# Kernel optimization log

Hardware: AMD Instinct MI355X
Metric: run time of the kernel (lower is better)

The kernel has to match this reference:

```python
import jax, jax.numpy as jnp
import numpy as np

H = 4  # heads (init_kwargs)
E = 64  # embed_size
D = E // H
PREC_DIM = 2
FF = 4 * E


def _layernorm(x, g, b, eps=1e-5):
    mu = jnp.mean(x, axis=-1, keepdims=True)
    var = jnp.mean((x - mu) ** 2, axis=-1, keepdims=True)
    return (x - mu) * jax.lax.rsqrt(var + eps) * g + b


def setup_inputs() -> dict:
    key = jax.random.key(0)
    ks = jax.random.split(key, 16)
    B, S, N = 128, 192, 32
    s = 0.05
    return {
        "precedence": jax.random.normal(ks[0], (B, S, N, PREC_DIM), dtype=jnp.float32),
        "top_mask": jax.random.randint(ks[1], (B, N), 0, 2, dtype=jnp.int32),
        "We": jax.random.normal(ks[2], (PREC_DIM, E), dtype=jnp.float32) * s,
        "be": jnp.zeros((E,), jnp.float32),
        "Wq": jax.random.normal(ks[3], (D, D), dtype=jnp.float32) * s,
        "Wk": jax.random.normal(ks[4], (D, D), dtype=jnp.float32) * s,
        "Wv": jax.random.normal(ks[5], (D, D), dtype=jnp.float32) * s,
        "Wo": jax.random.normal(ks[6], (E, E), dtype=jnp.float32) * s,
        "bo": jnp.zeros((E,), jnp.float32),
        "ln1_g": jnp.ones((E,), jnp.float32),
        "ln1_b": jnp.zeros((E,), jnp.float32),
        "W1": jax.random.normal(ks[7], (E, FF), dtype=jnp.float32) * s,
        "b1": jnp.zeros((FF,), jnp.float32),
        "W2": jax.random.normal(ks[8], (FF, E), dtype=jnp.float32) * s,
        "b2": jnp.zeros((E,), jnp.float32),
        "ln2_g": jnp.ones((E,), jnp.float32),
        "ln2_b": jnp.zeros((E,), jnp.float32),
    }


def reference(precedence, top_mask, We, be, Wq, Wk, Wv, Wo, bo,
              ln1_g, ln1_b, W1, b1, W2, b2, ln2_g, ln2_b):
    B, S, N, _ = precedence.shape
    M = B * S
    # embedding: [B,S,N,E]
    pv = precedence @ We + be
    # gather-indexed query: prec_vecs[:, s, s % box_num]
    sidx = jnp.arange(S)
    q = pv[:, sidx, sidx % N]                      # [B,S,E]
    vals = pv.reshape(M, N, E)                     # values == keys
    qr = q.reshape(M, 1, E)
    # mask: [B,1,1,N] expanded over states -> [M,1,1,N]
    mask = jnp.broadcast_to(top_mask[:, None, None, None, :], (B, S, 1, 1, N)).reshape(M, 1, 1, N)
    # per-head linear projections (shared across heads)
    vh = vals.reshape(M, N, H, D) @ Wv
    kh = vals.reshape(M, N, H, D) @ Wk
    qh = qr.reshape(M, 1, H, D) @ Wq
    energy = jnp.einsum("mqhd,mkhd->mhqk", qh, kh)           # [M,H,1,N]
    energy = jnp.where(mask == 0, jnp.float32(-1e20), energy)
    attn = jax.nn.softmax(energy / jnp.sqrt(jnp.float32(E)), axis=-1)
    oh = jnp.einsum("mhqk,mkhd->mqhd", attn, vh).reshape(M, 1, E)
    ao = oh @ Wo + bo
    x = _layernorm(ao + qr, ln1_g, ln1_b)
    ff = jax.nn.relu(x @ W1 + b1) @ W2 + b2
    out = _layernorm(ff + x, ln2_g, ln2_b)
    return out.reshape(B, S, E)
```

## Files before the change

### kernel.cpp

```cpp
#include <hip/hip_runtime.h>
#include <math.h>

namespace {

constexpr int S_  = 192;
constexpr int TPW = 8;
constexpr int WVB = 4;

__device__ __forceinline__ void wave_fence() {
  asm volatile("s_waitcnt lgkmcnt(0)" ::: "memory");
}

__launch_bounds__(256, 4)
__global__ void prec_fused(
    const float* __restrict__ prec,  const int*   __restrict__ tmask,
    const float* __restrict__ We,    const float* __restrict__ be,
    const float* __restrict__ Wq,    const float* __restrict__ Wk,
    const float* __restrict__ Wv,    const float* __restrict__ Wo,
    const float* __restrict__ bo,    const float* __restrict__ g1,
    const float* __restrict__ bb1,   const float* __restrict__ W1,
    const float* __restrict__ b1,    const float* __restrict__ W2,
    const float* __restrict__ b2,    const float* __restrict__ g2,
    const float* __restrict__ bb2,   float* __restrict__ out)
{
  __shared__ __align__(16) float scratch[WVB][2048];
  __shared__ __align__(16) float sxoh[WVB][TPW][64];

  const int tid  = threadIdx.x;
  const int wv   = tid >> 6;
  const int lane = tid & 63;
  const int u    = lane >> 5;
  const int n    = lane & 31;
  const int tokbase = (blockIdx.x * WVB + wv) * TPW;
  const int bidx0 = tokbase / S_;
  const int srow0 = tokbase - bidx0 * S_;

  float* __restrict__ sc = scratch[wv];

  const bool masked = (tmask[bidx0 * 32 + n] == 0);

  sc[lane]       = We[lane];
  sc[64 + lane]  = We[64 + lane];
  sc[128 + lane] = be[lane];
  #pragma unroll
  for (int i = 0; i < 4; ++i) {
    sc[192 + lane + 64*i] = Wq[lane + 64*i];
    sc[448 + lane + 64*i] = Wk[lane + 64*i];
    sc[704 + lane + 64*i] = Wv[lane + 64*i];
  }
  wave_fence();

  {
    const int h = lane >> 4, c = lane & 15;
    float Te[3] = {0,0,0}, Ke[3] = {0,0,0}, Ve[3] = {0,0,0};
    #pragma unroll
    for (int dp = 0; dp < 16; ++dp) {
      const float u0 = sc[h*16 + dp];
      const float u1 = sc[64 + h*16 + dp];
      const float u2 = sc[128 + h*16 + dp];
      const float wq = sc[192 + dp*16 + c];
      const float wk = sc[448 + dp*16 + c];
      const float wvv = sc[704 + dp*16 + c];
      Te[0] = fmaf(u0, wq, Te[0]); Te[1] = fmaf(u1, wq, Te[1]); Te[2] = fmaf(u2, wq, Te[2]);
      Ke[0] = fmaf(u0, wk, Ke[0]); Ke[1] = fmaf(u1, wk, Ke[1]); Ke[2] = fmaf(u2, wk, Ke[2]);
      Ve[0] = fmaf(u0, wvv, Ve[0]); Ve[1] = fmaf(u1, wvv, Ve[1]); Ve[2] = fmaf(u2, wvv, Ve[2]);
    }
    float Mp[9];
    #pragma unroll
    for (int a = 0; a < 3; ++a)
      #pragma unroll
      for (int b = 0; b < 3; ++b)
        Mp[a*3+b] = Te[a] * Ke[b];
    #pragma unroll
    for (int o = 1; o < 16; o <<= 1) {
      #pragma unroll
      for (int i = 0; i < 9; ++i) Mp[i] += __shfl_xor(Mp[i], o, 64);
    }
    #pragma unroll
    for (int a = 0; a < 3; ++a) sc[960 + (h*3 + a)*16 + c] = Ve[a];
    if (c == 0) {
      #pragma unroll
      for (int i = 0; i < 9; ++i) sc[1152 + h*9 + i] = Mp[i];
    }
  }
  wave_fence();

  float m0[9], m1[9];
  #pragma unroll
  for (int i = 0; i < 9; ++i) {
    m0[i] = sc[1152 + (2*u)*9 + i];
    m1[i] = sc[1152 + (2*u + 1)*9 + i];
  }
  float gO0[3] = {0,0,0}, gO1[3] = {0,0,0}, gT0[3] = {0,0,0}, gT1[3] = {0,0,0};
  {
    const int hoA = 2*u, hoB = 2*u + 1, htA = 2*(1 - u), htB = htA + 1;
    #pragma unroll
    for (int dp = 0; dp < 16; ++dp) {
      const float woA = Wo[(hoA*16 + dp)*64 + lane];
      const float woB = Wo[(hoB*16 + dp)*64 + lane];
      const float woC = Wo[(htA*16 + dp)*64 + lane];
      const float woD = Wo[(htB*16 + dp)*64 + lane];
      #pragma unroll
      for (int a = 0; a < 3; ++a) {
        gO0[a] = fmaf(sc[960 + (hoA*3 + a)*16 + dp], woA, gO0[a]);
        gO1[a] = fmaf(sc[960 + (hoB*3 + a)*16 + dp], woB, gO1[a]);
        gT0[a] = fmaf(sc[960 + (htA*3 + a)*16 + dp], woC, gT0[a]);
        gT1[a] = fmaf(sc[960 + (htB*3 + a)*16 + dp], woD, gT1[a]);
      }
    }
  }
  const float we0l = sc[lane], we1l = sc[64 + lane], bel = sc[128 + lane];
  const float bo_l = bo[lane], g1l = g1[lane], b1l_ = bb1[lane];
  wave_fence();

  #pragma unroll 1
  for (int p = 0; p < TPW; ++p) {
    const int m     = tokbase + p;
    const int nstar = (srow0 + p) & 31;

    const float qx = prec[(size_t)m * 64 + nstar * 2];
    const float qy = prec[(size_t)m * 64 + nstar * 2 + 1];
    const float2 pin = *(const float2*)(prec + (size_t)m * 64 + n * 2);

    const float cA0 = fmaf(qy, m0[3], fmaf(qx, m0[0], m0[6]));
    const float cB0 = fmaf(qy, m0[4], fmaf(qx, m0[1], m0[7]));
    const float cC0 = fmaf(qy, m0[5], fmaf(qx, m0[2], m0[8]));
    const float cA1 = fmaf(qy, m1[3], fmaf(qx, m1[0], m1[6]));
    const float cB1 = fmaf(qy, m1[4], fmaf(qx, m1[1], m1[7]));
    const float cC1 = fmaf(qy, m1[5], fmaf(qx, m1[2], m1[8]));

    const float en0 = fmaf(pin.y, cB0, fmaf(pin.x, cA0, cC0)) * 0.125f;
    const float en1 = fmaf(pin.y, cB1, fmaf(pin.x, cA1, cC1)) * 0.125f;

    const float pe0 = masked ? 0.f : __expf(en0);
    const float pe1 = masked ? 0.f : __expf(en1);
    float s0 = pe0, s1 = pe1;
    #pragma unroll
    for (int o = 1; o < 32; o <<= 1) {
      s0 += __shfl_xor(s0, o, 64);
      s1 += __shfl_xor(s1, o, 64);
    }
    const float w0 = (s0 > 0.f) ? pe0 / s0 : 0.03125f;
    const float w1 = (s1 > 0.f) ? pe1 / s1 : 0.03125f;

    float r0 = w0 * pin.x, r1 = w0 * pin.y, r2 = w0;
    float r3 = w1 * pin.x, r4 = w1 * pin.y, r5 = w1;
    #pragma unroll
    for (int o = 1; o < 32; o <<= 1) {
      r0 += __shfl_xor(r0, o, 64); r1 += __shfl_xor(r1, o, 64);
      r2 += __shfl_xor(r2, o, 64); r3 += __shfl_xor(r3, o, 64);
      r4 += __shfl_xor(r4, o, 64); r5 += __shfl_xor(r5, o, 64);
    }
    const float o0 = __shfl_xor(r0, 32, 64), o1 = __shfl_xor(r1, 32, 64);
    const float o2 = __shfl_xor(r2, 32, 64), o3 = __shfl_xor(r3, 32, 64);
    const float o4 = __shfl_xor(r4, 32, 64), o5 = __shfl_xor(r5, 32, 64);

    float v = bo_l;
    v = fmaf(r0, gO0[0], v); v = fmaf(r1, gO0[1], v); v = fmaf(r2, gO0[2], v);
    v = fmaf(r3, gO1[0], v); v = fmaf(r4, gO1[1], v); v = fmaf(r5, gO1[2], v);
    v = fmaf(o0, gT0[0], v); v = fmaf(o1, gT0[1], v); v = fmaf(o2, gT0[2], v);
    v = fmaf(o3, gT1[0], v); v = fmaf(o4, gT1[1], v); v = fmaf(o5, gT1[2], v);
    v += fmaf(qy, we1l, fmaf(qx, we0l, bel));

    float sm = v, s2 = v * v;
    #pragma unroll
    for (int o = 1; o < 64; o <<= 1) {
      sm += __shfl_xor(sm, o, 64);
      s2 += __shfl_xor(s2, o, 64);
    }
    const float mu  = sm * (1.f/64.f);
    const float var = s2 * (1.f/64.f) - mu * mu;
    const float rs  = rsqrtf(var + 1e-5f);
    sxoh[wv][p][lane] = (v - mu) * rs * g1l + b1l_;
  }
  wave_fence();

  float hacc[TPW][4];
  #pragma unroll
  for (int k = 0; k < 4; ++k) {
    const float bk = b1[lane + 64*k];
    #pragma unroll
    for (int t = 0; t < TPW; ++t) hacc[t][k] = bk;
  }
  #pragma unroll 4
  for (int e4 = 0; e4 < 16; ++e4) {
    float wr[4][4];
    #pragma unroll
    for (int kk = 0; kk < 4; ++kk)
      #pragma unroll
      for (int k = 0; k < 4; ++k)
        wr[kk][k] = W1[(e4*4 + kk)*256 + lane + 64*k];
    #pragma unroll
    for (int t = 0; t < TPW; ++t) {
      const float4 xv = *(const float4*)&sxoh[wv][t][e4*4];
      #pragma unroll
      for (int k = 0; k < 4; ++k) {
        hacc[t][k] = fmaf(xv.x, wr[0][k], hacc[t][k]);
        hacc[t][k] = fmaf(xv.y, wr[1][k], hacc[t][k]);
        hacc[t][k] = fmaf(xv.z, wr[2][k], hacc[t][k]);
        hacc[t][k] = fmaf(xv.w, wr[3][k], hacc[t][k]);
      }
    }
  }
  float* __restrict__ h1buf = sc;
  #pragma unroll
  for (int t = 0; t < TPW; ++t)
    #pragma unroll
    for (int k = 0; k < 4; ++k)
      h1buf[t*256 + lane + 64*k] = fmaxf(hacc[t][k], 0.f);
  wave_fence();

  const int tg = lane >> 5;
  const int e0 = (lane & 31) * 2;
  float f2a[4][2];
  {
    const float2 b2v = *(const float2*)(b2 + e0);
    #pragma unroll
    for (int i = 0; i < 4; ++i) { f2a[i][0] = b2v.x; f2a[i][1] = b2v.y; }
  }
  const float* __restrict__ hb = h1buf + tg * 4 * 256;
  #pragma unroll 8
  for (int f4 = 0; f4 < 64; ++f4) {
    float4 hv[4];
    #pragma unroll
    for (int i = 0; i < 4; ++i)
      hv[i] = *(const float4*)(hb + i*256 + f4*4);
    float2 w2r[4];
    #pragma unroll
    for (int ff = 0; ff < 4; ++ff)
      w2r[ff] = *(const float2*)(W2 + (f4*4 + ff)*64 + e0);
    #pragma unroll
    for (int i = 0; i < 4; ++i) {
      f2a[i][0] = fmaf(hv[i].x, w2r[0].x, f2a[i][0]);
      f2a[i][1] = fmaf(hv[i].x, w2r[0].y, f2a[i][1]);
      f2a[i][0] = fmaf(hv[i].y, w2r[1].x, f2a[i][0]);
      f2a[i][1] = fmaf(hv[i].y, w2r[1].y, f2a[i][1]);
      f2a[i][0] = fmaf(hv[i].z, w2r[2].x, f2a[i][0]);
      f2a[i][1] = fmaf(hv[i].z, w2r[2].y, f2a[i][1]);
      f2a[i][0] = fmaf(hv[i].w, w2r[3].x, f2a[i][0]);
      f2a[i][1] = fmaf(hv[i].w, w2r[3].y, f2a[i][1]);
    }
  }

  {
    const float2 g2v  = *(const float2*)(g2 + e0);
    const float2 bb2v = *(const float2*)(bb2 + e0);
    #pragma unroll
    for (int i = 0; i < 4; ++i) {
      const int t = tg * 4 + i;
      const float2 xv = *(const float2*)&sxoh[wv][t][e0];
      const float v0 = f2a[i][0] + xv.x;
      const float v1 = f2a[i][1] + xv.y;
      float sm = v0 + v1, s2 = v0*v0 + v1*v1;
      #pragma unroll
      for (int o = 1; o < 32; o <<= 1) {
        sm += __shfl_xor(sm, o, 64);
        s2 += __shfl_xor(s2, o, 64);
      }
      const float mu  = sm * (1.f/64.f);
      const float var = s2 * (1.f/64.f) - mu * mu;
      const float rs  = rsqrtf(var + 1e-5f);
      float2 o2;
      o2.x = (v0 - mu) * rs * g2v.x + bb2v.x;
      o2.y = (v1 - mu) * rs * g2v.y + bb2v.y;
      *(float2*)(out + (size_t)(tokbase + t) * 64 + e0) = o2;
    }
  }
}

}

extern "C" void kernel_launch(void* const* d_in, const int* in_sizes, int n_in,
                              void* d_out, int out_size, void* d_ws, size_t ws_size,
                              hipStream_t stream) {
  (void)in_sizes; (void)n_in; (void)d_ws; (void)ws_size; (void)out_size;
  const float* prec = (const float*)d_in[0];
  const int*   tm   = (const int*)  d_in[1];
  const float* We   = (const float*)d_in[2];
  const float* be   = (const float*)d_in[3];
  const float* Wq   = (const float*)d_in[4];
  const float* Wk   = (const float*)d_in[5];
  const float* Wv   = (const float*)d_in[6];
  const float* Wo   = (const float*)d_in[7];
  const float* bo   = (const float*)d_in[8];
  const float* g1   = (const float*)d_in[9];
  const float* bb1  = (const float*)d_in[10];
  const float* W1   = (const float*)d_in[11];
  const float* b1   = (const float*)d_in[12];
  const float* W2   = (const float*)d_in[13];
  const float* b2   = (const float*)d_in[14];
  const float* g2   = (const float*)d_in[15];
  const float* bb2  = (const float*)d_in[16];

  dim3 grid(768), block(256);
  hipLaunchKernelGGL(prec_fused, grid, block, 0, stream,
                     prec, tm, We, be, Wq, Wk, Wv, Wo, bo, g1, bb1,
                     W1, b1, W2, b2, g2, bb2, (float*)d_out);
}
```

Before: 143.5 us.

## Halve tokens per wave, share weight precompute across block, defer softmax normalization

Tokens per wave drop from 8 to 4, the grid doubles, and launch bounds target 6 blocks per CU with a smaller shared buffer, to raise occupancy. The per-wave redundant computation of the folded Q/K/V/Wo weights now runs once per block, split across all 256 threads and joined with __syncthreads. Softmax normalization moves after the reductions using reciprocals of the summed weights, and the bias term for the constant component is folded into one constant, which removes the separate sum shuffle. The new path adds block-level barriers and a uniform all-masked branch, and uses approximate reciprocals.

```diff
diff --git a/kernel.cpp b/kernel.cpp
--- a/kernel.cpp
+++ b/kernel.cpp
@@ -4,14 +4,14 @@
 namespace {
 
 constexpr int S_  = 192;
-constexpr int TPW = 8;
+constexpr int TPW = 4;
 constexpr int WVB = 4;
 
 __device__ __forceinline__ void wave_fence() {
   asm volatile("s_waitcnt lgkmcnt(0)" ::: "memory");
 }
 
-__launch_bounds__(256, 4)
+__launch_bounds__(256, 6)
 __global__ void prec_fused(
     const float* __restrict__ prec,  const int*   __restrict__ tmask,
     const float* __restrict__ We,    const float* __restrict__ be,
@@ -23,7 +23,7 @@
     const float* __restrict__ b2,    const float* __restrict__ g2,
     const float* __restrict__ bb2,   float* __restrict__ out)
 {
-  __shared__ __align__(16) float scratch[WVB][2048];
+  __shared__ __align__(16) float sh[WVB][1040];
   __shared__ __align__(16) float sxoh[WVB][TPW][64];
 
   const int tid  = threadIdx.x;
@@ -35,85 +35,84 @@
   const int bidx0 = tokbase / S_;
   const int srow0 = tokbase - bidx0 * S_;
 
-  float* __restrict__ sc = scratch[wv];
-
+  float* __restrict__ sc = &sh[0][0];
+
+  if (tid < 64) { sc[tid] = We[tid]; sc[64 + tid] = We[64 + tid]; sc[128 + tid] = be[tid]; }
+  sc[192 + tid] = Wq[tid];
+  sc[448 + tid] = Wk[tid];
+  sc[704 + tid] = Wv[tid];
+  __syncthreads();
+
+  {
+    const int sel = tid >> 6;
+    if (sel < 3) {
+      const int h = (tid >> 4) & 3, c = tid & 15;
+      const float* Wm = sc + 192 + sel * 256;
+      float a0 = 0.f, a1 = 0.f, a2 = 0.f;
+      #pragma unroll
+      for (int dp = 0; dp < 16; ++dp) {
+        const float w = Wm[dp * 16 + c];
+        a0 = fmaf(sc[h * 16 + dp],        w, a0);
+        a1 = fmaf(sc[64 + h * 16 + dp],   w, a1);
+        a2 = fmaf(sc[128 + h * 16 + dp],  w, a2);
+      }
+      const int base = 960 + sel * 192 + h * 48 + c;
+      sc[base] = a0; sc[base + 16] = a1; sc[base + 32] = a2;
+    }
+  }
+  __syncthreads();
+
+  if (tid < 36) {
+    const int h = tid / 9, ab = tid - h * 9, a = ab / 3, b = ab - a * 3;
+    const float* Tp = sc + 960  + h * 48 + a * 16;
+    const float* Kp = sc + 1152 + h * 48 + b * 16;
+    float s = 0.f;
+    #pragma unroll
+    for (int c = 0; c < 16; ++c) s = fmaf(Tp[c], Kp[c], s);
+    sc[1536 + tid] = s;
+  }
+  {
+    const int e = tid & 63, h = tid >> 6;
+    const float* Vp = sc + 1344 + h * 48;
+    float q0 = 0.f, q1 = 0.f, q2 = 0.f;
+    #pragma unroll
+    for (int dp = 0; dp < 16; ++dp) {
+      const float wo = Wo[(h * 16 + dp) * 64 + e];
+      q0 = fmaf(Vp[dp],      wo, q0);
+      q1 = fmaf(Vp[16 + dp], wo, q1);
+      q2 = fmaf(Vp[32 + dp], wo, q2);
+    }
+    sc[1600 + (h * 3 + 0) * 64 + e] = q0;
+    sc[1600 + (h * 3 + 1) * 64 + e] = q1;
+    sc[1600 + (h * 3 + 2) * 64 + e] = q2;
+  }
+  __syncthreads();
+
+  float m0[9], m1[9];
+  #pragma unroll
+  for (int i = 0; i < 9; ++i) {
+    m0[i] = sc[1536 + (2 * u) * 9 + i];
+    m1[i] = sc[1536 + (2 * u + 1) * 9 + i];
+  }
+  const int hoA = 2 * u, hoB = 2 * u + 1, htA = 2 - 2 * u, htB = 3 - 2 * u;
+  float gO0[2], gO1[2], gT0[2], gT1[2];
+  #pragma unroll
+  for (int a = 0; a < 2; ++a) {
+    gO0[a] = sc[1600 + (hoA * 3 + a) * 64 + lane];
+    gO1[a] = sc[1600 + (hoB * 3 + a) * 64 + lane];
+    gT0[a] = sc[1600 + (htA * 3 + a) * 64 + lane];
+    gT1[a] = sc[1600 + (htB * 3 + a) * 64 + lane];
+  }
+  float c0 = bo[lane];
+  #pragma unroll
+  for (int h = 0; h < 4; ++h) c0 += sc[1600 + (h * 3 + 2) * 64 + lane];
+  const float we0l = sc[lane], we1l = sc[64 + lane], bel = sc[128 + lane];
+  const float g1l = g1[lane], b1l_ = bb1[lane];
   const bool masked = (tmask[bidx0 * 32 + n] == 0);
-
-  sc[lane]       = We[lane];
-  sc[64 + lane]  = We[64 + lane];
-  sc[128 + lane] = be[lane];
-  #pragma unroll
-  for (int i = 0; i < 4; ++i) {
-    sc[192 + lane + 64*i] = Wq[lane + 64*i];
-    sc[448 + lane + 64*i] = Wk[lane + 64*i];
-    sc[704 + lane + 64*i] = Wv[lane + 64*i];
-  }
-  wave_fence();
-
-  {
-    const int h = lane >> 4, c = lane & 15;
-    float Te[3] = {0,0,0}, Ke[3] = {0,0,0}, Ve[3] = {0,0,0};
-    #pragma unroll
-    for (int dp = 0; dp < 16; ++dp) {
-      const float u0 = sc[h*16 + dp];
-      const float u1 = sc[64 + h*16 + dp];
-      const float u2 = sc[128 + h*16 + dp];
-      const float wq = sc[192 + dp*16 + c];
-      const float wk = sc[448 + dp*16 + c];
-      const float wvv = sc[704 + dp*16 + c];
-      Te[0] = fmaf(u0, wq, Te[0]); Te[1] = fmaf(u1, wq, Te[1]); Te[2] = fmaf(u2, wq, Te[2]);
-      Ke[0] = fmaf(u0, wk, Ke[0]); Ke[1] = fmaf(u1, wk, Ke[1]); Ke[2] = fmaf(u2, wk, Ke[2]);
-      Ve[0] = fmaf(u0, wvv, Ve[0]); Ve[1] = fmaf(u1, wvv, Ve[1]); Ve[2] = fmaf(u2, wvv, Ve[2]);
-    }
-    float Mp[9];
-    #pragma unroll
-    for (int a = 0; a < 3; ++a)
-      #pragma unroll
-      for (int b = 0; b < 3; ++b)
-        Mp[a*3+b] = Te[a] * Ke[b];
-    #pragma unroll
-    for (int o = 1; o < 16; o <<= 1) {
-      #pragma unroll
-      for (int i = 0; i < 9; ++i) Mp[i] += __shfl_xor(Mp[i], o, 64);
-    }
-    #pragma unroll
-    for (int a = 0; a < 3; ++a) sc[960 + (h*3 + a)*16 + c] = Ve[a];
-    if (c == 0) {
-      #pragma unroll
-      for (int i = 0; i < 9; ++i) sc[1152 + h*9 + i] = Mp[i];
-    }
-  }
-  wave_fence();
-
-  float m0[9], m1[9];
-  #pragma unroll
-  for (int i = 0; i < 9; ++i) {
-    m0[i] = sc[1152 + (2*u)*9 + i];
-    m1[i] = sc[1152 + (2*u + 1)*9 + i];
-  }
-  float gO0[3] = {0,0,0}, gO1[3] = {0,0,0}, gT0[3] = {0,0,0}, gT1[3] = {0,0,0};
-  {
-    const int hoA = 2*u, hoB = 2*u + 1, htA = 2*(1 - u), htB = htA + 1;
-    #pragma unroll
-    for (int dp = 0; dp < 16; ++dp) {
-      const float woA = Wo[(hoA*16 + dp)*64 + lane];
-      const float woB = Wo[(hoB*16 + dp)*64 + lane];
-      const float woC = Wo[(htA*16 + dp)*64 + lane];
-      const float woD = Wo[(htB*16 + dp)*64 + lane];
-      #pragma unroll
-      for (int a = 0; a < 3; ++a) {
-        gO0[a] = fmaf(sc[960 + (hoA*3 + a)*16 + dp], woA, gO0[a]);
-        gO1[a] = fmaf(sc[960 + (hoB*3 + a)*16 + dp], woB, gO1[a]);
-        gT0[a] = fmaf(sc[960 + (htA*3 + a)*16 + dp], woC, gT0[a]);
-        gT1[a] = fmaf(sc[960 + (htB*3 + a)*16 + dp], woD, gT1[a]);
-      }
-    }
-  }
-  const float we0l = sc[lane], we1l = sc[64 + lane], bel = sc[128 + lane];
-  const float bo_l = bo[lane], g1l = g1[lane], b1l_ = bb1[lane];
-  wave_fence();
-
-  #pragma unroll 1
+  const bool allm   = (__all((int)masked) != 0);
+  __syncthreads();
+
+  #pragma unroll 2
   for (int p = 0; p < TPW; ++p) {
     const int m     = tokbase + p;
     const int nstar = (srow0 + p) & 31;
@@ -128,23 +127,18 @@
     const float cA1 = fmaf(qy, m1[3], fmaf(qx, m1[0], m1[6]));
     const float cB1 = fmaf(qy, m1[4], fmaf(qx, m1[1], m1[7]));
     const float cC1 = fmaf(qy, m1[5], fmaf(qx, m1[2], m1[8]));
-
     const float en0 = fmaf(pin.y, cB0, fmaf(pin.x, cA0, cC0)) * 0.125f;
     const float en1 = fmaf(pin.y, cB1, fmaf(pin.x, cA1, cC1)) * 0.125f;
 
-    const float pe0 = masked ? 0.f : __expf(en0);
-    const float pe1 = masked ? 0.f : __expf(en1);
-    float s0 = pe0, s1 = pe1;
-    #pragma unroll
-    for (int o = 1; o < 32; o <<= 1) {
-      s0 += __shfl_xor(s0, o, 64);
-      s1 += __shfl_xor(s1, o, 64);
-    }
-    const float w0 = (s0 > 0.f) ? pe0 / s0 : 0.03125f;
-    const float w1 = (s1 > 0.f) ? pe1 / s1 : 0.03125f;
-
-    float r0 = w0 * pin.x, r1 = w0 * pin.y, r2 = w0;
-    float r3 = w1 * pin.x, r4 = w1 * pin.y, r5 = w1;
+    float pe0, pe1;
+    if (allm) { pe0 = 1.f; pe1 = 1.f; }
+    else {
+      pe0 = masked ? 0.f : __expf(en0);
+      pe1 = masked ? 0.f : __expf(en1);
+    }
+
+    float r0 = pe0 * pin.x, r1 = pe0 * pin.y, r2 = pe0;
+    float r3 = pe1 * pin.x, r4 = pe1 * pin.y, r5 = pe1;
     #pragma unroll
     for (int o = 1; o < 32; o <<= 1) {
       r0 += __shfl_xor(r0, o, 64); r1 += __shfl_xor(r1, o, 64);
@@ -154,12 +148,14 @@
     const float o0 = __shfl_xor(r0, 32, 64), o1 = __shfl_xor(r1, 32, 64);
     const float o2 = __shfl_xor(r2, 32, 64), o3 = __shfl_xor(r3, 32, 64);
     const float o4 = __shfl_xor(r4, 32, 64), o5 = __shfl_xor(r5, 32, 64);
-
-    float v = bo_l;
-    v = fmaf(r0, gO0[0], v); v = fmaf(r1, gO0[1], v); v = fmaf(r2, gO0[2], v);
-    v = fmaf(r3, gO1[0], v); v = fmaf(r4, gO1[1], v); v = fmaf(r5, gO1[2], v);
-    v = fmaf(o0, gT0[0], v); v = fmaf(o1, gT0[1], v); v = fmaf(o2, gT0[2], v);
-    v = fmaf(o3, gT1[0], v); v = fmaf(o4, gT1[1], v); v = fmaf(o5, gT1[2], v);
+    const float i0 = __builtin_amdgcn_rcpf(r2), i1 = __builtin_amdgcn_rcpf(r5);
+    const float i2 = __builtin_amdgcn_rcpf(o2), i3 = __builtin_amdgcn_rcpf(o5);
+
+    float v = c0;
+    v = fmaf(fmaf(r1, gO0[1], r0 * gO0[0]), i0, v);
+    v = fmaf(fmaf(r4, gO1[1], r3 * gO1[0]), i1, v);
+    v = fmaf(fmaf(o1, gT0[1], o0 * gT0[0]), i2, v);
+    v = fmaf(fmaf(o4, gT1[1], o3 * gT1[0]), i3, v);
     v += fmaf(qy, we1l, fmaf(qx, we0l, bel));
 
     float sm = v, s2 = v * v;
@@ -168,8 +164,8 @@
       sm += __shfl_xor(sm, o, 64);
       s2 += __shfl_xor(s2, o, 64);
     }
-    const float mu  = sm * (1.f/64.f);
-    const float var = s2 * (1.f/64.f) - mu * mu;
+    const float mu  = sm * (1.f / 64.f);
+    const float var = s2 * (1.f / 64.f) - mu * mu;
     const float rs  = rsqrtf(var + 1e-5f);
     sxoh[wv][p][lane] = (v - mu) * rs * g1l + b1l_;
   }
@@ -178,7 +174,7 @@
   float hacc[TPW][4];
   #pragma unroll
   for (int k = 0; k < 4; ++k) {
-    const float bk = b1[lane + 64*k];
+    const float bk = b1[lane + 64 * k];
     #pragma unroll
     for (int t = 0; t < TPW; ++t) hacc[t][k] = bk;
   }
@@ -189,10 +185,10 @@
     for (int kk = 0; kk < 4; ++kk)
       #pragma unroll
       for (int k = 0; k < 4; ++k)
-        wr[kk][k] = W1[(e4*4 + kk)*256 + lane + 64*k];
+        wr[kk][k] = W1[(e4 * 4 + kk) * 256 + lane + 64 * k];
     #pragma unroll
     for (int t = 0; t < TPW; ++t) {
-      const float4 xv = *(const float4*)&sxoh[wv][t][e4*4];
+      const float4 xv = *(const float4*)&sxoh[wv][t][e4 * 4];
       #pragma unroll
       for (int k = 0; k < 4; ++k) {
         hacc[t][k] = fmaf(xv.x, wr[0][k], hacc[t][k]);
@@ -202,63 +198,58 @@
       }
     }
   }
-  float* __restrict__ h1buf = sc;
+  float* __restrict__ h1buf = sh[wv];
   #pragma unroll
   for (int t = 0; t < TPW; ++t)
     #pragma unroll
     for (int k = 0; k < 4; ++k)
-      h1buf[t*256 + lane + 64*k] = fmaxf(hacc[t][k], 0.f);
+      h1buf[t * 256 + lane + 64 * k] = fmaxf(hacc[t][k], 0.f);
   wave_fence();
 
   const int tg = lane >> 5;
   const int e0 = (lane & 31) * 2;
-  float f2a[4][2];
+  float f2a[2][2];
   {
     const float2 b2v = *(const float2*)(b2 + e0);
-    #pragma unroll
-    for (int i = 0; i < 4; ++i) { f2a[i][0] = b2v.x; f2a[i][1] = b2v.y; }
-  }
-  const float* __restrict__ hb = h1buf + tg * 4 * 256;
+    f2a[0][0] = b2v.x; f2a[0][1] = b2v.y;
+    f2a[1][0] = b2v.x; f2a[1][1] = b2v.y;
+  }
+  const float* __restrict__ hb = h1buf + tg * 2 * 256;
   #pragma unroll 8
   for (int f4 = 0; f4 < 64; ++f4) {
-    float4 hv[4];
-    #pragma unroll
-    for (int i = 0; i < 4; ++i)
-      hv[i] = *(const float4*)(hb + i*256 + f4*4);
-    float2 w2r[4];
-    #pragma unroll
-    for (int ff = 0; ff < 4; ++ff)
-      w2r[ff] = *(const float2*)(W2 + (f4*4 + ff)*64 + e0);
-    #pragma unroll
-    for (int i = 0; i < 4; ++i) {
-      f2a[i][0] = fmaf(hv[i].x, w2r[0].x, f2a[i][0]);
-      f2a[i][1] = fmaf(hv[i].x, w2r[0].y, f2a[i][1]);
-      f2a[i][0] = fmaf(hv[i].y, w2r[1].x, f2a[i][0]);
-      f2a[i][1] = fmaf(hv[i].y, w2r[1].y, f2a[i][1]);
-      f2a[i][0] = fmaf(hv[i].z, w2r[2].x, f2a[i][0]);
-      f2a[i][1] = fmaf(hv[i].z, w2r[2].y, f2a[i][1]);
-      f2a[i][0] = fmaf(hv[i].w, w2r[3].x, f2a[i][0]);
-      f2a[i][1] = fmaf(hv[i].w, w2r[3].y, f2a[i][1]);
-    }
+    const float4 hv0 = *(const float4*)(hb + f4 * 4);
+    const float4 hv1 = *(const float4*)(hb + 256 + f4 * 4);
+    const float2 w0 = *(const float2*)(W2 + (f4 * 4 + 0) * 64 + e0);
+    const float2 w1 = *(const float2*)(W2 + (f4 * 4 + 1) * 64 + e0);
+    const float2 w2 = *(const float2*)(W2 + (f4 * 4 + 2) * 64 + e0);
+    const float2 w3 = *(const float2*)(W2 + (f4 * 4 + 3) * 64 + e0);
+    f2a[0][0] = fmaf(hv0.x, w0.x, f2a[0][0]); f2a[0][1] = fmaf(hv0.x, w0.y, f2a[0][1]);
+    f2a[0][0] = fmaf(hv0.y, w1.x, f2a[0][0]); f2a[0][1] = fmaf(hv0.y, w1.y, f2a[0][1]);
+    f2a[0][0] = fmaf(hv0.z, w2.x, f2a[0][0]); f2a[0][1] = fmaf(hv0.z, w2.y, f2a[0][1]);
+    f2a[0][0] = fmaf(hv0.w, w3.x, f2a[0][0]); f2a[0][1] = fmaf(hv0.w, w3.y, f2a[0][1]);
+    f2a[1][0] = fmaf(hv1.x, w0.x, f2a[1][0]); f2a[1][1] = fmaf(hv1.x, w0.y, f2a[1][1]);
+    f2a[1][0] = fmaf(hv1.y, w1.x, f2a[1][0]); f2a[1][1] = fmaf(hv1.y, w1.y, f2a[1][1]);
+    f2a[1][0] = fmaf(hv1.z, w2.x, f2a[1][0]); f2a[1][1] = fmaf(hv1.z, w2.y, f2a[1][1]);
+    f2a[1][0] = fmaf(hv1.w, w3.x, f2a[1][0]); f2a[1][1] = fmaf(hv1.w, w3.y, f2a[1][1]);
   }
 
   {
     const float2 g2v  = *(const float2*)(g2 + e0);
     const float2 bb2v = *(const float2*)(bb2 + e0);
     #pragma unroll
-    for (int i = 0; i < 4; ++i) {
-      const int t = tg * 4 + i;
+    for (int i = 0; i < 2; ++i) {
+      const int t = tg * 2 + i;
       const float2 xv = *(const float2*)&sxoh[wv][t][e0];
       const float v0 = f2a[i][0] + xv.x;
       const float v1 = f2a[i][1] + xv.y;
-      float sm = v0 + v1, s2 = v0*v0 + v1*v1;
+      float sm = v0 + v1, s2 = v0 * v0 + v1 * v1;
       #pragma unroll
       for (int o = 1; o < 32; o <<= 1) {
         sm += __shfl_xor(sm, o, 64);
         s2 += __shfl_xor(s2, o, 64);
       }
-      const float mu  = sm * (1.f/64.f);
-      const float var = s2 * (1.f/64.f) - mu * mu;
+      const float mu  = sm * (1.f / 64.f);
+      const float var = s2 * (1.f / 64.f) - mu * mu;
       const float rs  = rsqrtf(var + 1e-5f);
       float2 o2;
       o2.x = (v0 - mu) * rs * g2v.x + bb2v.x;
@@ -292,7 +283,7 @@
   const float* g2   = (const float*)d_in[15];
   const float* bb2  = (const float*)d_in[16];
 
-  dim3 grid(768), block(256);
+  dim3 grid(1536), block(256);
   hipLaunchKernelGGL(prec_fused, grid, block, 0, stream,
                      prec, tm, We, be, Wq, Wk, Wv, Wo, bo, g1, bb1,
                      W1, b1, W2, b2, g2, bb2, (float*)d_out);
```

Result: slower. 155.0 us (+8.0%).
